# Optimization experiments

Measured on AMD Instinct MI355X. Metric: run time of the kernel, lower is better.

Reference implementation:

```python
import jax, jax.numpy as jnp
import numpy as np


def conv2d_same(x, w, b=None):
    # x: [B,C,H,W], w: [O,I,kh,kw], stride 1, SAME padding (pad=1 for 3x3)
    out = jax.lax.conv_general_dilated(
        x, w, window_strides=(1, 1), padding='SAME',
        dimension_numbers=('NCHW', 'OIHW', 'NCHW'))
    if b is not None:
        out = out + b[None, :, None, None]
    return out


def deform_conv(x, offset, wd, k=3, pad=1, dg=4):
    # DCNv1: per-location offset-guided bilinear sampling + weighted accumulation.
    # x: [B,C,H,W]; offset: [B, dg*k*k*2, H, W] as (dy,dx) pairs per kernel tap;
    # wd: [O, C, k, k] (bias-free, as in mmcv DeformConv).
    B, C, H, W = x.shape
    cg = C // dg          # channels per deformable group
    K = k * k
    off = offset.reshape(B, dg, K, 2, H, W)
    dy, dx = off[:, :, :, 0], off[:, :, :, 1]          # [B,dg,K,H,W]
    ky = (jnp.arange(K) // k - pad).astype(x.dtype)    # kernel row offsets
    kx = (jnp.arange(K) % k - pad).astype(x.dtype)     # kernel col offsets
    hh = jnp.arange(H, dtype=x.dtype)
    ww = jnp.arange(W, dtype=x.dtype)
    py = dy + ky[None, None, :, None, None] + hh[None, None, None, :, None]
    px = dx + kx[None, None, :, None, None] + ww[None, None, None, None, :]
    y0 = jnp.floor(py); x0 = jnp.floor(px)
    wy1 = py - y0; wy0 = 1.0 - wy1
    wx1 = px - x0; wx0 = 1.0 - wx1
    xg = x.reshape(B, dg, cg, H * W)

    def gather(yi, xi):
        # zero outside the feature map (implicit zero padding of bilinear kernel)
        valid = (yi >= 0) & (yi < H) & (xi >= 0) & (xi < W)
        yc = jnp.clip(yi, 0, H - 1).astype(jnp.int32)
        xc = jnp.clip(xi, 0, W - 1).astype(jnp.int32)
        idx = (yc * W + xc).reshape(B, dg, 1, K * H * W)
        g = jnp.take_along_axis(xg, jnp.broadcast_to(idx, (B, dg, cg, K * H * W)), axis=-1)
        g = g.reshape(B, dg, cg, K, H, W)
        return g * valid[:, :, None].astype(x.dtype)

    val = (gather(y0, x0) * (wy0 * wx0)[:, :, None]
           + gather(y0, x0 + 1) * (wy0 * wx1)[:, :, None]
           + gather(y0 + 1, x0) * (wy1 * wx0)[:, :, None]
           + gather(y0 + 1, x0 + 1) * (wy1 * wx1)[:, :, None])  # [B,dg,cg,K,H,W]
    wr = wd.reshape(wd.shape[0], dg, cg, K)
    return jnp.einsum('ogck,bgckhw->bohw', wr, val)


def setup_inputs() -> dict:
    key = jax.random.key(0)
    k1, k2, k3, k4 = jax.random.split(key, 4)
    B, C, H, W = 8, 256, 64, 64
    dg, ks = 4, 3
    x = jax.random.normal(k1, (B, C, H, W), dtype=jnp.float32)
    w1 = jax.random.normal(k2, (C, C, 3, 3), dtype=jnp.float32) * 0.01
    b1 = jnp.zeros((C,), dtype=jnp.float32)
    w2 = jax.random.normal(k3, (dg * ks * ks * 2, C, 3, 3), dtype=jnp.float32) * 0.01
    b2 = jnp.zeros((dg * ks * ks * 2,), dtype=jnp.float32)
    wd = jax.random.normal(k4, (C, C, ks, ks), dtype=jnp.float32) * 0.01
    return {'x': x, 'w1': w1, 'b1': b1, 'w2': w2, 'b2': b2, 'wd': wd}


def reference(x, w1, b1, w2, b2, wd):
    # offset branch uses x.detach() in the original
    xd = jax.lax.stop_gradient(x)
    offset = conv2d_same(conv2d_same(xd, w1, b1), w2, b2)
    return jax.nn.relu(deform_conv(x, offset, wd, k=3, pad=1, dg=4))
```

## Files before the change

kernel.cpp:

```cpp
#include <hip/hip_runtime.h>
#include <hip/hip_bf16.h>


typedef __attribute__((ext_vector_type(8))) short bf16x8;
typedef __attribute__((ext_vector_type(4))) float f32x4;

static __device__ __forceinline__ ushort f2bf(float f) {
  __hip_bfloat16 h = __float2bfloat16(f);
  return *reinterpret_cast<ushort*>(&h);
}
static __device__ __forceinline__ float bf2f(ushort u) {
  union { uint u32; float f; } cv;
  cv.u32 = ((uint)u) << 16;
  return cv.f;
}

__global__ __launch_bounds__(256) void prep_weights(
    const float* __restrict__ w1, const float* __restrict__ w2,
    const float* __restrict__ wd,
    ushort* __restrict__ wt1s, ushort* __restrict__ wt2s,
    ushort* __restrict__ wtds) {
  const int N1 = 36 * 256 * 64;
  const int N2 = 36 * 80 * 64;
  const int N3 = 36 * 256 * 64;
  int total = N1 + N2 + N3;
  for (int i = blockIdx.x * 256 + threadIdx.x; i < total; i += gridDim.x * 256) {
    if (i < N1) {
      int e = i & 7, p = (i >> 3) & 7, co = (i >> 6) & 255, ti = i >> 14;
      int cc = ((p ^ (co & 7)) << 3) + e;
      int kk = ti >> 2, chunk = ti & 3;
      wt1s[i] = f2bf(w1[(co * 256 + chunk * 64 + cc) * 9 + kk]);
    } else if (i < N1 + N2) {
      int d = i - N1;
      int e = d & 7, p = (d >> 3) & 7;
      int r = d >> 6;
      int co = r % 80, ti = r / 80;
      int cc = ((p ^ (co & 7)) << 3) + e;
      int kk = ti >> 2, chunk = ti & 3;
      wt2s[d] = (co < 72) ? f2bf(w2[(co * 256 + chunk * 64 + cc) * 9 + kk])
                          : (ushort)0;
    } else {
      int d = i - N1 - N2;
      int e = d & 7, p = (d >> 3) & 7, co = (d >> 6) & 255, ti = d >> 14;
      int c = ((p ^ (co & 7)) << 3) + e;
      int g = ti / 9, kk = ti - g * 9;
      wtds[d] = f2bf(wd[(co * 256 + g * 64 + c) * 9 + kk]);
    }
  }
}

__global__ __launch_bounds__(256) void transpose_x(
    const float* __restrict__ x, ushort* __restrict__ xt) {
  int id = blockIdx.x;
  int y = id & 63, bg = id >> 6;
  int c = threadIdx.x & 63, xi = threadIdx.x >> 6;
  const float* ip = x + (((size_t)bg) << 18) + ((size_t)c << 12) + y * 64;
  ushort* op = xt + (((size_t)bg) << 18) + (size_t)y * 4096 + c;
#pragma unroll
  for (int j = 0; j < 16; ++j) {
    int xx = xi * 16 + j;
    op[(size_t)xx * 64] = f2bf(ip[xx]);
  }
}

template <int MODE, int NFR, bool RELU, bool HASBIAS, bool OUT_CHLAST>
__global__ __launch_bounds__(256, 2) void fa_mfma6(
    const ushort* __restrict__ inT,
    const float* __restrict__ off,
    const char* __restrict__ wBs,
    const float* __restrict__ bias,
    void* __restrict__ outp,
    int co_total, int co_write) {
  constexpr int CO_TILE = NFR * 16;
  constexpr int TILE_B = CO_TILE * 128;
  constexpr int NCALLS = (TILE_B + 4095) / 4096;
  constexpr int NRN = (MODE == 1) ? 8 : 2;
  __shared__ __align__(16) ushort Blds[2][NCALLS * 2048];

  int id = blockIdx.x;
  int id2 = (id & 7) * 64 + (id >> 3);
  int b = id2 >> 6, h = id2 & 63;
  int t = threadIdx.x;
  int wv = t >> 6, lane = t & 63;
  int ml = lane & 15, kc = lane >> 4;
  int ml7 = ml & 7;

  auto stage = [&](int ti, int bufsel) {
#pragma unroll
    for (int m = 0; m < NCALLS; ++m) {
      int d = (m * 256 + t) * 16;
      int ds = (d > TILE_B - 16) ? (TILE_B - 16) : d;
      const char* src = wBs + (size_t)ti * TILE_B + ds;
      ushort* dst = &Blds[bufsel][(m * 256 + t) * 8];
      __builtin_amdgcn_global_load_lds(
          (const __attribute__((address_space(1))) void*)src,
          (__attribute__((address_space(3))) void*)dst, 16, 0, 0);
    }
  };

  const int pcol = wv * 16 + ml;

  const bf16x8 bz = {0, 0, 0, 0, 0, 0, 0, 0};
  bf16x8 aCur[2];
  bf16x8 rN[NRN];
  float wsv[4];
  float2 offA;

  auto issueA0 = [&](int tn) {
    int kk = tn >> 2, chunk = tn & 3;
    int ky = kk / 3, kx = kk - ky * 3;
    int gy = h + ky - 1, gx = pcol + kx - 1;
    bool inb = (gy >= 0) & (gy < 64) & (gx >= 0) & (gx < 64);
    const ushort* p =
        inT + ((((size_t)(b * 4 + chunk) << 12) + gy * 64 + gx) << 6) + kc * 8;
    rN[0] = bz;
    rN[1] = bz;
    if (inb) {
      rN[0] = *(const bf16x8*)p;
      rN[1] = *(const bf16x8*)(p + 32);
    }
  };
  auto finishA0 = [&]() {
    aCur[0] = rN[0];
    aCur[1] = rN[1];
  };

  auto loadOff = [&](int tn) {
    int g = tn / 9, kk = tn - 9 * (tn / 9);
    int ch = g * 18 + kk * 2;
    const float* offp = off + (((size_t)b * 72 + ch) << 12) + h * 64 + pcol;
    offA.x = offp[0];
    offA.y = offp[4096];
  };
  auto issueA1 = [&](int tn) {
    int g = tn / 9, kk = tn - 9 * (tn / 9);
    int ky = kk / 3, kx = kk - ky * 3;
    const ushort* base = inT + (((size_t)(b * 4 + g)) << 18) + kc * 8;
    float py = (float)(h + ky - 1) + offA.x;
    float pxf = (float)(pcol + kx - 1) + offA.y;
    float y0f = floorf(py), x0f = floorf(pxf);
    float wy1 = py - y0f, wx1 = pxf - x0f;
    float wy0 = 1.f - wy1, wx0 = 1.f - wx1;
    int y0 = (int)y0f, x0i = (int)x0f;
    int y1 = y0 + 1, x1i = x0i + 1;
    bool vy0 = (y0 >= 0) & (y0 < 64);
    bool vy1 = (y1 >= 0) & (y1 < 64);
    bool vx0 = (x0i >= 0) & (x0i < 64);
    bool vx1 = (x1i >= 0) & (x1i < 64);
    wsv[0] = (vy0 & vx0) ? wy0 * wx0 : 0.f;
    wsv[1] = (vy0 & vx1) ? wy0 * wx1 : 0.f;
    wsv[2] = (vy1 & vx0) ? wy1 * wx0 : 0.f;
    wsv[3] = (vy1 & vx1) ? wy1 * wx1 : 0.f;
    int yc0 = min(max(y0, 0), 63), yc1 = min(max(y1, 0), 63);
    int xc0 = min(max(x0i, 0), 63), xc1 = min(max(x1i, 0), 63);
    const ushort* p00 = base + ((yc0 * 64 + xc0) << 6);
    const ushort* p01 = base + ((yc0 * 64 + xc1) << 6);
    const ushort* p10 = base + ((yc1 * 64 + xc0) << 6);
    const ushort* p11 = base + ((yc1 * 64 + xc1) << 6);
    rN[0] = *(const bf16x8*)p00;
    rN[1] = *(const bf16x8*)(p00 + 32);
    rN[2] = *(const bf16x8*)p01;
    rN[3] = *(const bf16x8*)(p01 + 32);
    rN[4] = *(const bf16x8*)p10;
    rN[5] = *(const bf16x8*)(p10 + 32);
    rN[6] = *(const bf16x8*)p11;
    rN[7] = *(const bf16x8*)(p11 + 32);
  };
  auto finishA1 = [&]() {
    float w00 = wsv[0], w01 = wsv[1], w10 = wsv[2], w11 = wsv[3];
#pragma unroll
    for (int ks = 0; ks < 2; ++ks) {
      bf16x8 q00 = rN[0 + ks], q01 = rN[2 + ks];
      bf16x8 q10 = rN[4 + ks], q11 = rN[6 + ks];
      bf16x8 av;
#pragma unroll
      for (int jj = 0; jj < 4; ++jj) {
        float v0 = w00 * bf2f((ushort)q00[2 * jj]) + w01 * bf2f((ushort)q01[2 * jj]) +
                   w10 * bf2f((ushort)q10[2 * jj]) + w11 * bf2f((ushort)q11[2 * jj]);
        float v1 = w00 * bf2f((ushort)q00[2 * jj + 1]) + w01 * bf2f((ushort)q01[2 * jj + 1]) +
                   w10 * bf2f((ushort)q10[2 * jj + 1]) + w11 * bf2f((ushort)q11[2 * jj + 1]);
        av[2 * jj] = (short)f2bf(v0);
        av[2 * jj + 1] = (short)f2bf(v1);
      }
      aCur[ks] = av;
    }
  };

  f32x4 acc[NFR];
#pragma unroll
  for (int j = 0; j < NFR; ++j) acc[j] = (f32x4){0.f, 0.f, 0.f, 0.f};

  if (MODE == 1) {
    loadOff(0);
    issueA1(0);
    loadOff(1);
    finishA1();
  } else {
    issueA0(0);
    finishA0();
  }
  stage(0, 0);
  __syncthreads();

  for (int ti = 0; ti < 36; ++ti) {
    int cur = ti & 1;
    if (ti < 35) {
      stage(ti + 1, cur ^ 1);
      if (MODE == 1) issueA1(ti + 1); else issueA0(ti + 1);
    }
    if (MODE == 1 && ti < 34) loadOff(ti + 2);

#pragma unroll
    for (int ks = 0; ks < 2; ++ks) {
      int sw = (((ks * 4 + kc) ^ ml7) << 3);
      bf16x8 bq[NFR];
#pragma unroll
      for (int nf = 0; nf < NFR; ++nf)
        bq[nf] = *(const bf16x8*)&Blds[cur][(nf * 16 + ml) * 64 + sw];
#pragma unroll
      for (int nf = 0; nf < NFR; ++nf)
        acc[nf] = __builtin_amdgcn_mfma_f32_16x16x32_bf16(
            aCur[ks], bq[nf], acc[nf], 0, 0, 0);
    }

    if (ti < 35) { if (MODE == 1) finishA1(); else finishA0(); }
    __syncthreads();
  }

  int rq = lane >> 4;
#pragma unroll
  for (int nf = 0; nf < NFR; ++nf) {
    int cog = nf * 16 + ml;
    if (cog < co_write) {
      float bv = HASBIAS ? bias[cog] : 0.f;
#pragma unroll
      for (int ri = 0; ri < 4; ++ri) {
        int pxe = wv * 16 + rq * 4 + ri;
        float v = acc[nf][ri] + bv;
        if (RELU) v = fmaxf(v, 0.f);
        if (OUT_CHLAST) {
          int g_out = cog >> 6, ci = cog & 63;
          ((ushort*)outp)[((((size_t)(b * 4 + g_out) << 12) + h * 64 + pxe) << 6) + ci] =
              f2bf(v);
        } else {
          ((float*)outp)[(((size_t)b * co_total + cog) << 12) + h * 64 + pxe] = v;
        }
      }
    }
  }
}

extern "C" void kernel_launch(void* const* d_in, const int* in_sizes, int n_in,
                              void* d_out, int out_size, void* d_ws, size_t ws_size,
                              hipStream_t stream) {
  const float* x  = (const float*)d_in[0];
  const float* w1 = (const float*)d_in[1];
  const float* b1 = (const float*)d_in[2];
  const float* w2 = (const float*)d_in[3];
  const float* b2 = (const float*)d_in[4];
  const float* wd = (const float*)d_in[5];

  char* wsb = (char*)d_ws;
  float*  off_buf = (float*)wsb;
  ushort* xt      = (ushort*)(wsb + 9437184);
  ushort* wt1s    = (ushort*)(wsb + 26214400);
  ushort* wt2s    = (ushort*)(wsb + 27394048);
  ushort* wtds    = (ushort*)(wsb + 27762688);

  prep_weights<<<2048, 256, 0, stream>>>(w1, w2, wd, wt1s, wt2s, wtds);
  transpose_x<<<2048, 256, 0, stream>>>(x, xt);

  fa_mfma6<0, 16, false, true, true>
      <<<512, 256, 0, stream>>>(xt, nullptr, (const char*)wt1s, b1, d_out, 256, 256);

  fa_mfma6<0, 5, false, true, false>
      <<<512, 256, 0, stream>>>((const ushort*)d_out, nullptr, (const char*)wt2s,
                                b2, off_buf, 72, 72);

  fa_mfma6<1, 16, true, false, false>
      <<<512, 256, 0, stream>>>(xt, off_buf, (const char*)wtds, nullptr, d_out,
                                256, 256);
}
```

Baseline: 189.1 us.

## Split K dimension across blocks with bf16 partials and separate reduce kernels

Each conv/deform-conv kernel now uses 512-thread blocks covering two output rows, and splits the 36 K-steps into two halves handled by different blocks. Each half writes bf16 partial sums to a workspace buffer, and three new reduce kernels combine them and apply bias, ReLU and the final layout transpose. The kernel also raises wave priority around the MFMA section. In exchange it adds extra launches and partial-buffer traffic, and storing partials in bf16 loses accuracy.

```diff
diff --git a/kernel.cpp b/kernel.cpp
--- a/kernel.cpp
+++ b/kernel.cpp
@@ -63,42 +63,47 @@
   }
 }
 
-template <int MODE, int NFR, bool RELU, bool HASBIAS, bool OUT_CHLAST>
-__global__ __launch_bounds__(256, 2) void fa_mfma6(
+template <int MODE, int NFR, bool CHLAST>
+__global__ __launch_bounds__(512, 4) void fa_mfma8(
     const ushort* __restrict__ inT,
     const float* __restrict__ off,
     const char* __restrict__ wBs,
-    const float* __restrict__ bias,
-    void* __restrict__ outp,
-    int co_total, int co_write) {
+    ushort* __restrict__ parA,
+    ushort* __restrict__ parB,
+    int co_write) {
   constexpr int CO_TILE = NFR * 16;
   constexpr int TILE_B = CO_TILE * 128;
-  constexpr int NCALLS = (TILE_B + 4095) / 4096;
+  constexpr int NCALLS = (TILE_B + 8191) / 8192;
   constexpr int NRN = (MODE == 1) ? 8 : 2;
-  __shared__ __align__(16) ushort Blds[2][NCALLS * 2048];
+  __shared__ __align__(16) ushort Blds[2][NCALLS * 4096];
 
   int id = blockIdx.x;
   int id2 = (id & 7) * 64 + (id >> 3);
-  int b = id2 >> 6, h = id2 & 63;
+  int khalf = id2 & 1;
+  int rest = id2 >> 1;
+  int hp = rest & 31, b = rest >> 5;
   int t = threadIdx.x;
   int wv = t >> 6, lane = t & 63;
   int ml = lane & 15, kc = lane >> 4;
   int ml7 = ml & 7;
-
-  auto stage = [&](int ti, int bufsel) {
+  ushort* par = khalf ? parB : parA;
+
+  auto stage = [&](int tg, int bufsel) {
 #pragma unroll
     for (int m = 0; m < NCALLS; ++m) {
-      int d = (m * 256 + t) * 16;
+      int d = (m * 512 + t) * 16;
       int ds = (d > TILE_B - 16) ? (TILE_B - 16) : d;
-      const char* src = wBs + (size_t)ti * TILE_B + ds;
-      ushort* dst = &Blds[bufsel][(m * 256 + t) * 8];
+      const char* src = wBs + (size_t)tg * TILE_B + ds;
+      ushort* dst = &Blds[bufsel][(m * 512 + t) * 8];
       __builtin_amdgcn_global_load_lds(
           (const __attribute__((address_space(1))) void*)src,
           (__attribute__((address_space(3))) void*)dst, 16, 0, 0);
     }
   };
 
-  const int pcol = wv * 16 + ml;
+  const int pxll = wv * 16 + ml;
+  const int row = hp * 2 + (pxll >> 6);
+  const int col = pxll & 63;
 
   const bf16x8 bz = {0, 0, 0, 0, 0, 0, 0, 0};
   bf16x8 aCur[2];
@@ -106,10 +111,10 @@
   float wsv[4];
   float2 offA;
 
-  auto issueA0 = [&](int tn) {
-    int kk = tn >> 2, chunk = tn & 3;
+  auto issueA0 = [&](int tg) {
+    int kk = tg >> 2, chunk = tg & 3;
     int ky = kk / 3, kx = kk - ky * 3;
-    int gy = h + ky - 1, gx = pcol + kx - 1;
+    int gy = row + ky - 1, gx = col + kx - 1;
     bool inb = (gy >= 0) & (gy < 64) & (gx >= 0) & (gx < 64);
     const ushort* p =
         inT + ((((size_t)(b * 4 + chunk) << 12) + gy * 64 + gx) << 6) + kc * 8;
@@ -125,19 +130,19 @@
     aCur[1] = rN[1];
   };
 
-  auto loadOff = [&](int tn) {
-    int g = tn / 9, kk = tn - 9 * (tn / 9);
+  auto loadOff = [&](int tg) {
+    int g = tg / 9, kk = tg - 9 * (tg / 9);
     int ch = g * 18 + kk * 2;
-    const float* offp = off + (((size_t)b * 72 + ch) << 12) + h * 64 + pcol;
+    const float* offp = off + (((size_t)b * 72 + ch) << 12) + row * 64 + col;
     offA.x = offp[0];
     offA.y = offp[4096];
   };
-  auto issueA1 = [&](int tn) {
-    int g = tn / 9, kk = tn - 9 * (tn / 9);
+  auto issueA1 = [&](int tg) {
+    int g = tg / 9, kk = tg - 9 * (tg / 9);
     int ky = kk / 3, kx = kk - ky * 3;
     const ushort* base = inT + (((size_t)(b * 4 + g)) << 18) + kc * 8;
-    float py = (float)(h + ky - 1) + offA.x;
-    float pxf = (float)(pcol + kx - 1) + offA.y;
+    float py = (float)(row + ky - 1) + offA.x;
+    float pxf = (float)(col + kx - 1) + offA.y;
     float y0f = floorf(py), x0f = floorf(pxf);
     float wy1 = py - y0f, wx1 = pxf - x0f;
     float wy0 = 1.f - wy1, wx0 = 1.f - wx1;
@@ -190,26 +195,30 @@
 #pragma unroll
   for (int j = 0; j < NFR; ++j) acc[j] = (f32x4){0.f, 0.f, 0.f, 0.f};
 
+  const int t0 = khalf * 18;
+
   if (MODE == 1) {
-    loadOff(0);
-    issueA1(0);
-    loadOff(1);
+    loadOff(t0);
+    issueA1(t0);
+    loadOff(t0 + 1);
     finishA1();
   } else {
-    issueA0(0);
+    issueA0(t0);
     finishA0();
   }
-  stage(0, 0);
+  stage(t0, 0);
   __syncthreads();
 
-  for (int ti = 0; ti < 36; ++ti) {
-    int cur = ti & 1;
-    if (ti < 35) {
-      stage(ti + 1, cur ^ 1);
-      if (MODE == 1) issueA1(ti + 1); else issueA0(ti + 1);
-    }
-    if (MODE == 1 && ti < 34) loadOff(ti + 2);
-
+  for (int tloc = 0; tloc < 18; ++tloc) {
+    int tg = t0 + tloc;
+    int cur = tloc & 1;
+    if (tloc < 17) {
+      stage(tg + 1, cur ^ 1);
+      if (MODE == 1) issueA1(tg + 1); else issueA0(tg + 1);
+    }
+    if (MODE == 1 && tloc < 16) loadOff(tg + 2);
+
+    __builtin_amdgcn_s_setprio(1);
 #pragma unroll
     for (int ks = 0; ks < 2; ++ks) {
       int sw = (((ks * 4 + kc) ^ ml7) << 3);
@@ -222,8 +231,9 @@
         acc[nf] = __builtin_amdgcn_mfma_f32_16x16x32_bf16(
             aCur[ks], bq[nf], acc[nf], 0, 0, 0);
     }
-
-    if (ti < 35) { if (MODE == 1) finishA1(); else finishA0(); }
+    __builtin_amdgcn_s_setprio(0);
+
+    if (tloc < 17) { if (MODE == 1) finishA1(); else finishA0(); }
     __syncthreads();
   }
 
@@ -232,21 +242,86 @@
   for (int nf = 0; nf < NFR; ++nf) {
     int cog = nf * 16 + ml;
     if (cog < co_write) {
-      float bv = HASBIAS ? bias[cog] : 0.f;
 #pragma unroll
       for (int ri = 0; ri < 4; ++ri) {
-        int pxe = wv * 16 + rq * 4 + ri;
-        float v = acc[nf][ri] + bv;
-        if (RELU) v = fmaxf(v, 0.f);
-        if (OUT_CHLAST) {
-          int g_out = cog >> 6, ci = cog & 63;
-          ((ushort*)outp)[((((size_t)(b * 4 + g_out) << 12) + h * 64 + pxe) << 6) + ci] =
-              f2bf(v);
+        int pix = hp * 128 + wv * 16 + rq * 4 + ri;
+        ushort v = f2bf(acc[nf][ri]);
+        if (CHLAST) {
+          par[((((size_t)(b * 4 + (cog >> 6)) << 12) + pix) << 6) + (cog & 63)] = v;
         } else {
-          ((float*)outp)[(((size_t)b * co_total + cog) << 12) + h * 64 + pxe] = v;
+          par[(((size_t)b * co_write + cog) << 12) + pix] = v;
         }
       }
     }
+  }
+}
+
+__global__ __launch_bounds__(256) void reduce_c1(
+    const ushort* __restrict__ p0, const ushort* __restrict__ p1,
+    const float* __restrict__ bias, ushort* __restrict__ t1) {
+  const int N8 = (8 * 4 * 4096 * 64) / 8;
+  for (int i = blockIdx.x * 256 + threadIdx.x; i < N8; i += gridDim.x * 256) {
+    size_t base = (size_t)i * 8;
+    bf16x8 a = *(const bf16x8*)(p0 + base);
+    bf16x8 c = *(const bf16x8*)(p1 + base);
+    int c0 = (int)(base & 63);
+    int g = (int)((base >> 18) & 3);
+    bf16x8 o;
+#pragma unroll
+    for (int j = 0; j < 8; ++j) {
+      float v = bf2f((ushort)a[j]) + bf2f((ushort)c[j]) + bias[g * 64 + c0 + j];
+      o[j] = (short)f2bf(v);
+    }
+    *(bf16x8*)(t1 + base) = o;
+  }
+}
+
+__global__ __launch_bounds__(256) void reduce_c2(
+    const ushort* __restrict__ p0, const ushort* __restrict__ p1,
+    const float* __restrict__ bias, float* __restrict__ out) {
+  const int N8 = (8 * 72 * 4096) / 8;
+  for (int i = blockIdx.x * 256 + threadIdx.x; i < N8; i += gridDim.x * 256) {
+    size_t base = (size_t)i * 8;
+    bf16x8 a = *(const bf16x8*)(p0 + base);
+    bf16x8 c = *(const bf16x8*)(p1 + base);
+    int co = (int)((base >> 12) % 72);
+    float bv = bias[co];
+    float4 o0, o1;
+    o0.x = bf2f((ushort)a[0]) + bf2f((ushort)c[0]) + bv;
+    o0.y = bf2f((ushort)a[1]) + bf2f((ushort)c[1]) + bv;
+    o0.z = bf2f((ushort)a[2]) + bf2f((ushort)c[2]) + bv;
+    o0.w = bf2f((ushort)a[3]) + bf2f((ushort)c[3]) + bv;
+    o1.x = bf2f((ushort)a[4]) + bf2f((ushort)c[4]) + bv;
+    o1.y = bf2f((ushort)a[5]) + bf2f((ushort)c[5]) + bv;
+    o1.z = bf2f((ushort)a[6]) + bf2f((ushort)c[6]) + bv;
+    o1.w = bf2f((ushort)a[7]) + bf2f((ushort)c[7]) + bv;
+    *(float4*)(out + base) = o0;
+    *(float4*)(out + base + 4) = o1;
+  }
+}
+
+__global__ __launch_bounds__(256) void reduce_df(
+    const ushort* __restrict__ p0, const ushort* __restrict__ p1,
+    float* __restrict__ out) {
+  __shared__ float ts[64][65];
+  int bid = blockIdx.x;
+  int pt = bid & 63, cq = (bid >> 6) & 3, b = bid >> 8;
+  int t = threadIdx.x;
+  int c = t & 63, ty = t >> 6;
+  size_t inbase = (((size_t)(b * 4 + cq) << 12) + pt * 64) << 6;
+#pragma unroll 4
+  for (int s = 0; s < 16; ++s) {
+    int pxi = ty * 16 + s;
+    size_t idx = inbase + ((size_t)pxi << 6) + c;
+    float v = bf2f(p0[idx]) + bf2f(p1[idx]);
+    ts[c][pxi] = fmaxf(v, 0.f);
+  }
+  __syncthreads();
+  int px = t & 63;
+#pragma unroll 4
+  for (int s = 0; s < 16; ++s) {
+    int coi = ty * 16 + s;
+    out[(((size_t)b * 256 + cq * 64 + coi) << 12) + pt * 64 + px] = ts[coi][px];
   }
 }
 
@@ -266,18 +341,23 @@
   ushort* wt1s    = (ushort*)(wsb + 26214400);
   ushort* wt2s    = (ushort*)(wsb + 27394048);
   ushort* wtds    = (ushort*)(wsb + 27762688);
+  ushort* par0    = (ushort*)(wsb + 28942336);
+  ushort* par1    = (ushort*)(wsb + 45719552);
 
   prep_weights<<<2048, 256, 0, stream>>>(w1, w2, wd, wt1s, wt2s, wtds);
   transpose_x<<<2048, 256, 0, stream>>>(x, xt);
 
-  fa_mfma6<0, 16, false, true, true>
-      <<<512, 256, 0, stream>>>(xt, nullptr, (const char*)wt1s, b1, d_out, 256, 256);
-
-  fa_mfma6<0, 5, false, true, false>
-      <<<512, 256, 0, stream>>>((const ushort*)d_out, nullptr, (const char*)wt2s,
-                                b2, off_buf, 72, 72);
-
-  fa_mfma6<1, 16, true, false, false>
-      <<<512, 256, 0, stream>>>(xt, off_buf, (const char*)wtds, nullptr, d_out,
-                                256, 256);
-}
+  ushort* t1 = (ushort*)d_out;
+
+  fa_mfma8<0, 16, true><<<512, 512, 0, stream>>>(
+      xt, nullptr, (const char*)wt1s, par0, par1, 256);
+  reduce_c1<<<2048, 256, 0, stream>>>(par0, par1, b1, t1);
+
+  fa_mfma8<0, 5, false><<<512, 512, 0, stream>>>(
+      t1, nullptr, (const char*)wt2s, par0, par1, 72);
+  reduce_c2<<<1024, 256, 0, stream>>>(par0, par1, b2, off_buf);
+
+  fa_mfma8<1, 16, true><<<512, 512, 0, stream>>>(
+      xt, off_buf, (const char*)wtds, par0, par1, 256);
+  reduce_df<<<2048, 256, 0, stream>>>(par0, par1, (float*)d_out);
+}
```

Result: slower. 208.8 us (+10.4%).

## Split reduction dimension across two blocks with partial buffers and reduce kernels

Applied to the files above, without the earlier changes.

Each GEMM-like kernel is split along the 36-step reduction into two halves, doubling the grid to 1024 blocks. Each half writes bf16 partial sums that new reduce kernels combine, adding bias and ReLU. Weight tiles are re-laid out into per-half-k sub-tiles without swizzle, shrinking LDS and allowing 3 blocks per SM, and MFMA sections are wrapped with setprio. The aim is more occupancy and parallelism at the cost of extra partial-sum traffic, three extra launches, and an extra bf16 rounding of the partial sums.

```diff
diff --git a/kernel.cpp b/kernel.cpp
--- a/kernel.cpp
+++ b/kernel.cpp
@@ -18,33 +18,34 @@
 __global__ __launch_bounds__(256) void prep_weights(
     const float* __restrict__ w1, const float* __restrict__ w2,
     const float* __restrict__ wd,
-    ushort* __restrict__ wt1s, ushort* __restrict__ wt2s,
-    ushort* __restrict__ wtds) {
-  const int N1 = 36 * 256 * 64;
-  const int N2 = 36 * 80 * 64;
-  const int N3 = 36 * 256 * 64;
+    ushort* __restrict__ wt1, ushort* __restrict__ wt2,
+    ushort* __restrict__ wtd) {
+  const int N1 = 72 * 4 * 256 * 8;
+  const int N2 = 72 * 4 * 128 * 8;
+  const int N3 = 72 * 4 * 256 * 8;
   int total = N1 + N2 + N3;
   for (int i = blockIdx.x * 256 + threadIdx.x; i < total; i += gridDim.x * 256) {
     if (i < N1) {
-      int e = i & 7, p = (i >> 3) & 7, co = (i >> 6) & 255, ti = i >> 14;
-      int cc = ((p ^ (co & 7)) << 3) + e;
-      int kk = ti >> 2, chunk = ti & 3;
-      wt1s[i] = f2bf(w1[(co * 256 + chunk * 64 + cc) * 9 + kk]);
+      int e = i & 7, co = (i >> 3) & 255, p = (i >> 11) & 3, tk = i >> 13;
+      int ti = tk >> 1, half = tk & 1;
+      int kk = ti >> 2, ch = ti & 3;
+      int cc = half * 32 + p * 8 + e;
+      wt1[i] = f2bf(w1[(co * 256 + ch * 64 + cc) * 9 + kk]);
     } else if (i < N1 + N2) {
       int d = i - N1;
-      int e = d & 7, p = (d >> 3) & 7;
-      int r = d >> 6;
-      int co = r % 80, ti = r / 80;
-      int cc = ((p ^ (co & 7)) << 3) + e;
-      int kk = ti >> 2, chunk = ti & 3;
-      wt2s[d] = (co < 72) ? f2bf(w2[(co * 256 + chunk * 64 + cc) * 9 + kk])
-                          : (ushort)0;
+      int e = d & 7, co = (d >> 3) & 127, p = (d >> 10) & 3, tk = d >> 12;
+      int ti = tk >> 1, half = tk & 1;
+      int kk = ti >> 2, ch = ti & 3;
+      int cc = half * 32 + p * 8 + e;
+      wt2[d] = (co < 72) ? f2bf(w2[(co * 256 + ch * 64 + cc) * 9 + kk])
+                         : (ushort)0;
     } else {
       int d = i - N1 - N2;
-      int e = d & 7, p = (d >> 3) & 7, co = (d >> 6) & 255, ti = d >> 14;
-      int c = ((p ^ (co & 7)) << 3) + e;
-      int g = ti / 9, kk = ti - g * 9;
-      wtds[d] = f2bf(wd[(co * 256 + g * 64 + c) * 9 + kk]);
+      int e = d & 7, co = (d >> 3) & 255, p = (d >> 11) & 3, tk = d >> 13;
+      int ti = tk >> 1, half = tk & 1;
+      int g = ti / 9, kkt = ti - g * 9;
+      int c = half * 32 + p * 8 + e;
+      wtd[d] = f2bf(wd[(co * 256 + g * 64 + c) * 9 + kkt]);
     }
   }
 }
@@ -63,51 +64,50 @@
   }
 }
 
-template <int MODE, int NFR, bool RELU, bool HASBIAS, bool OUT_CHLAST>
-__global__ __launch_bounds__(256, 2) void fa_mfma6(
+template <int MODE, int NFR>
+__global__ __launch_bounds__(256, 3) void fa_mfma10(
     const ushort* __restrict__ inT,
     const float* __restrict__ off,
-    const char* __restrict__ wBs,
-    const float* __restrict__ bias,
-    void* __restrict__ outp,
-    int co_total, int co_write) {
+    const ushort* __restrict__ wBs,
+    ushort* __restrict__ parA,
+    ushort* __restrict__ parB) {
   constexpr int CO_TILE = NFR * 16;
-  constexpr int TILE_B = CO_TILE * 128;
-  constexpr int NCALLS = (TILE_B + 4095) / 4096;
+  constexpr int SUB_U = CO_TILE * 32;
+  constexpr int NCALLS = (SUB_U * 2) / 4096;
   constexpr int NRN = (MODE == 1) ? 8 : 2;
-  __shared__ __align__(16) ushort Blds[2][NCALLS * 2048];
+  __shared__ __align__(16) ushort Blds[2][SUB_U];
 
   int id = blockIdx.x;
-  int id2 = (id & 7) * 64 + (id >> 3);
-  int b = id2 >> 6, h = id2 & 63;
+  int id2 = (id & 7) * 128 + (id >> 3);
+  int khalf = id2 & 1;
+  int rest = id2 >> 1;
+  int h = rest & 63, b = rest >> 6;
   int t = threadIdx.x;
   int wv = t >> 6, lane = t & 63;
   int ml = lane & 15, kc = lane >> 4;
-  int ml7 = ml & 7;
-
-  auto stage = [&](int ti, int bufsel) {
+  int pcol = wv * 16 + ml;
+  ushort* par = khalf ? parB : parA;
+
+  auto stage = [&](int s, int buf) {
+    int tk = khalf * 36 + s;
+    const char* src0 = (const char*)wBs + (size_t)tk * (SUB_U * 2) + t * 16;
+    ushort* dst0 = &Blds[buf][t * 8];
 #pragma unroll
     for (int m = 0; m < NCALLS; ++m) {
-      int d = (m * 256 + t) * 16;
-      int ds = (d > TILE_B - 16) ? (TILE_B - 16) : d;
-      const char* src = wBs + (size_t)ti * TILE_B + ds;
-      ushort* dst = &Blds[bufsel][(m * 256 + t) * 8];
       __builtin_amdgcn_global_load_lds(
-          (const __attribute__((address_space(1))) void*)src,
-          (__attribute__((address_space(3))) void*)dst, 16, 0, 0);
-    }
-  };
-
-  const int pcol = wv * 16 + ml;
+          (const __attribute__((address_space(1))) void*)(src0 + m * 4096),
+          (__attribute__((address_space(3))) void*)(dst0 + m * 2048), 16, 0, 0);
+    }
+  };
 
   const bf16x8 bz = {0, 0, 0, 0, 0, 0, 0, 0};
-  bf16x8 aCur[2];
+  bf16x8 aCur0, aCur1;
   bf16x8 rN[NRN];
   float wsv[4];
   float2 offA;
 
-  auto issueA0 = [&](int tn) {
-    int kk = tn >> 2, chunk = tn & 3;
+  auto issueA0 = [&](int tap) {
+    int kk = tap >> 2, chunk = tap & 3;
     int ky = kk / 3, kx = kk - ky * 3;
     int gy = h + ky - 1, gx = pcol + kx - 1;
     bool inb = (gy >= 0) & (gy < 64) & (gx >= 0) & (gx < 64);
@@ -121,20 +121,20 @@
     }
   };
   auto finishA0 = [&]() {
-    aCur[0] = rN[0];
-    aCur[1] = rN[1];
-  };
-
-  auto loadOff = [&](int tn) {
-    int g = tn / 9, kk = tn - 9 * (tn / 9);
-    int ch = g * 18 + kk * 2;
+    aCur0 = rN[0];
+    aCur1 = rN[1];
+  };
+
+  auto loadOff = [&](int tap) {
+    int g = tap / 9, kkt = tap - 9 * (tap / 9);
+    int ch = g * 18 + kkt * 2;
     const float* offp = off + (((size_t)b * 72 + ch) << 12) + h * 64 + pcol;
     offA.x = offp[0];
     offA.y = offp[4096];
   };
-  auto issueA1 = [&](int tn) {
-    int g = tn / 9, kk = tn - 9 * (tn / 9);
-    int ky = kk / 3, kx = kk - ky * 3;
+  auto issueA1 = [&](int tap) {
+    int g = tap / 9, kkt = tap - 9 * (tap / 9);
+    int ky = kkt / 3, kx = kkt - ky * 3;
     const ushort* base = inT + (((size_t)(b * 4 + g)) << 18) + kc * 8;
     float py = (float)(h + ky - 1) + offA.x;
     float pxf = (float)(pcol + kx - 1) + offA.y;
@@ -174,15 +174,12 @@
       bf16x8 q10 = rN[4 + ks], q11 = rN[6 + ks];
       bf16x8 av;
 #pragma unroll
-      for (int jj = 0; jj < 4; ++jj) {
-        float v0 = w00 * bf2f((ushort)q00[2 * jj]) + w01 * bf2f((ushort)q01[2 * jj]) +
-                   w10 * bf2f((ushort)q10[2 * jj]) + w11 * bf2f((ushort)q11[2 * jj]);
-        float v1 = w00 * bf2f((ushort)q00[2 * jj + 1]) + w01 * bf2f((ushort)q01[2 * jj + 1]) +
-                   w10 * bf2f((ushort)q10[2 * jj + 1]) + w11 * bf2f((ushort)q11[2 * jj + 1]);
-        av[2 * jj] = (short)f2bf(v0);
-        av[2 * jj + 1] = (short)f2bf(v1);
+      for (int jj = 0; jj < 8; ++jj) {
+        float v = w00 * bf2f((ushort)q00[jj]) + w01 * bf2f((ushort)q01[jj]) +
+                  w10 * bf2f((ushort)q10[jj]) + w11 * bf2f((ushort)q11[jj]);
+        av[jj] = (short)f2bf(v);
       }
-      aCur[ks] = av;
+      if (ks == 0) aCur0 = av; else aCur1 = av;
     }
   };
 
@@ -190,63 +187,122 @@
 #pragma unroll
   for (int j = 0; j < NFR; ++j) acc[j] = (f32x4){0.f, 0.f, 0.f, 0.f};
 
+  auto domfma = [&](bf16x8 a, int buf) {
+    __builtin_amdgcn_s_setprio(1);
+#pragma unroll
+    for (int nf = 0; nf < NFR; ++nf) {
+      bf16x8 bq = *(const bf16x8*)&Blds[buf][(kc * CO_TILE + nf * 16 + ml) * 8];
+      acc[nf] = __builtin_amdgcn_mfma_f32_16x16x32_bf16(a, bq, acc[nf], 0, 0, 0);
+    }
+    __builtin_amdgcn_s_setprio(0);
+  };
+
+  const int tap0 = khalf * 18;
+
   if (MODE == 1) {
-    loadOff(0);
-    issueA1(0);
-    loadOff(1);
+    loadOff(tap0);
+    issueA1(tap0);
+    loadOff(tap0 + 1);
     finishA1();
   } else {
-    issueA0(0);
+    issueA0(tap0);
     finishA0();
   }
   stage(0, 0);
   __syncthreads();
 
-  for (int ti = 0; ti < 36; ++ti) {
-    int cur = ti & 1;
-    if (ti < 35) {
-      stage(ti + 1, cur ^ 1);
-      if (MODE == 1) issueA1(ti + 1); else issueA0(ti + 1);
-    }
-    if (MODE == 1 && ti < 34) loadOff(ti + 2);
-
-#pragma unroll
-    for (int ks = 0; ks < 2; ++ks) {
-      int sw = (((ks * 4 + kc) ^ ml7) << 3);
-      bf16x8 bq[NFR];
-#pragma unroll
-      for (int nf = 0; nf < NFR; ++nf)
-        bq[nf] = *(const bf16x8*)&Blds[cur][(nf * 16 + ml) * 64 + sw];
-#pragma unroll
-      for (int nf = 0; nf < NFR; ++nf)
-        acc[nf] = __builtin_amdgcn_mfma_f32_16x16x32_bf16(
-            aCur[ks], bq[nf], acc[nf], 0, 0, 0);
-    }
-
-    if (ti < 35) { if (MODE == 1) finishA1(); else finishA0(); }
+  for (int tp = 0; tp < 18; ++tp) {
+    int tap = tap0 + tp;
+    if (2 * tp + 1 < 36) stage(2 * tp + 1, 1);
+    if (tp < 17) { if (MODE == 1) issueA1(tap + 1); else issueA0(tap + 1); }
+    if (MODE == 1 && tp < 16) loadOff(tap + 2);
+    domfma(aCur0, 0);
     __syncthreads();
-  }
-
-  int rq = lane >> 4;
-#pragma unroll
-  for (int nf = 0; nf < NFR; ++nf) {
-    int cog = nf * 16 + ml;
-    if (cog < co_write) {
-      float bv = HASBIAS ? bias[cog] : 0.f;
-#pragma unroll
-      for (int ri = 0; ri < 4; ++ri) {
-        int pxe = wv * 16 + rq * 4 + ri;
-        float v = acc[nf][ri] + bv;
-        if (RELU) v = fmaxf(v, 0.f);
-        if (OUT_CHLAST) {
-          int g_out = cog >> 6, ci = cog & 63;
-          ((ushort*)outp)[((((size_t)(b * 4 + g_out) << 12) + h * 64 + pxe) << 6) + ci] =
-              f2bf(v);
-        } else {
-          ((float*)outp)[(((size_t)b * co_total + cog) << 12) + h * 64 + pxe] = v;
-        }
-      }
-    }
+    if (2 * tp + 2 < 36) stage(2 * tp + 2, 0);
+    domfma(aCur1, 1);
+    if (tp < 17) { if (MODE == 1) finishA1(); else finishA0(); }
+    __syncthreads();
+  }
+
+  size_t wbase = ((size_t)((b * 64 + h) * 4 + wv)) * (NFR * 4 * 64);
+#pragma unroll
+  for (int nf = 0; nf < NFR; ++nf)
+#pragma unroll
+    for (int ri = 0; ri < 4; ++ri)
+      par[wbase + (nf * 4 + ri) * 64 + lane] = f2bf(acc[nf][ri]);
+}
+
+
+__global__ __launch_bounds__(256) void reduce_c1(
+    const ushort* __restrict__ p0, const ushort* __restrict__ p1,
+    const float* __restrict__ bias, ushort* __restrict__ t1) {
+  const int N = 8 * 4 * 4096 * 8;
+  for (int i = blockIdx.x * 256 + threadIdx.x; i < N; i += gridDim.x * 256) {
+    int cg = i & 7;
+    int pix = (i >> 3) & 4095;
+    int g = (i >> 15) & 3;
+    int b = i >> 17;
+    int h = pix >> 6, col = pix & 63;
+    int wv = col >> 4, rr = col & 15;
+    int rq = rr >> 2, ri = rr & 3;
+    int cp = g * 64 + cg * 8;
+    int nf = cp >> 4, mlb = cp & 15;
+    size_t idx = ((size_t)((b * 64 + h) * 4 + wv)) * 4096 +
+                 (nf * 4 + ri) * 64 + rq * 16 + mlb;
+    bf16x8 a = *(const bf16x8*)(p0 + idx);
+    bf16x8 c = *(const bf16x8*)(p1 + idx);
+    bf16x8 o;
+#pragma unroll
+    for (int j = 0; j < 8; ++j)
+      o[j] = (short)f2bf(bf2f((ushort)a[j]) + bf2f((ushort)c[j]) + bias[cp + j]);
+    *(bf16x8*)(t1 + ((size_t)(b * 4 + g) * 4096 + pix) * 64 + cg * 8) = o;
+  }
+}
+
+__global__ __launch_bounds__(256) void reduce_c2(
+    const ushort* __restrict__ p0, const ushort* __restrict__ p1,
+    const float* __restrict__ bias, float* __restrict__ out) {
+  const int N = 8 * 72 * 1024;
+  for (int i = blockIdx.x * 256 + threadIdx.x; i < N; i += gridDim.x * 256) {
+    int p4 = i & 1023;
+    int r = i >> 10;
+    int co = r % 72, b = r / 72;
+    int h = p4 >> 4;
+    int col0 = (p4 & 15) * 4;
+    int wv = col0 >> 4, rq = (col0 >> 2) & 3;
+    int nf = co >> 4, ml = co & 15;
+    size_t base = ((size_t)((b * 64 + h) * 4 + wv)) * 2048 +
+                  nf * 256 + rq * 16 + ml;
+    float bv = bias[co];
+    float4 o;
+    o.x = bf2f(p0[base +   0]) + bf2f(p1[base +   0]) + bv;
+    o.y = bf2f(p0[base +  64]) + bf2f(p1[base +  64]) + bv;
+    o.z = bf2f(p0[base + 128]) + bf2f(p1[base + 128]) + bv;
+    o.w = bf2f(p0[base + 192]) + bf2f(p1[base + 192]) + bv;
+    *(float4*)(out + (((size_t)b * 72 + co) << 12) + p4 * 4) = o;
+  }
+}
+
+__global__ __launch_bounds__(256) void reduce_df(
+    const ushort* __restrict__ p0, const ushort* __restrict__ p1,
+    float* __restrict__ out) {
+  const int N = 8 * 256 * 1024;
+  for (int i = blockIdx.x * 256 + threadIdx.x; i < N; i += gridDim.x * 256) {
+    int p4 = i & 1023;
+    int co = (i >> 10) & 255;
+    int b = i >> 18;
+    int h = p4 >> 4;
+    int col0 = (p4 & 15) * 4;
+    int wv = col0 >> 4, rq = (col0 >> 2) & 3;
+    int nf = co >> 4, ml = co & 15;
+    size_t base = ((size_t)((b * 64 + h) * 4 + wv)) * 4096 +
+                  nf * 256 + rq * 16 + ml;
+    float4 o;
+    o.x = fmaxf(bf2f(p0[base +   0]) + bf2f(p1[base +   0]), 0.f);
+    o.y = fmaxf(bf2f(p0[base +  64]) + bf2f(p1[base +  64]), 0.f);
+    o.z = fmaxf(bf2f(p0[base + 128]) + bf2f(p1[base + 128]), 0.f);
+    o.w = fmaxf(bf2f(p0[base + 192]) + bf2f(p1[base + 192]), 0.f);
+    *(float4*)(out + (((size_t)b * 256 + co) << 12) + p4 * 4) = o;
   }
 }
 
@@ -263,21 +319,23 @@
   char* wsb = (char*)d_ws;
   float*  off_buf = (float*)wsb;
   ushort* xt      = (ushort*)(wsb + 9437184);
-  ushort* wt1s    = (ushort*)(wsb + 26214400);
-  ushort* wt2s    = (ushort*)(wsb + 27394048);
-  ushort* wtds    = (ushort*)(wsb + 27762688);
-
-  prep_weights<<<2048, 256, 0, stream>>>(w1, w2, wd, wt1s, wt2s, wtds);
+  ushort* wt1     = (ushort*)(wsb + 26214400);
+  ushort* wt2     = (ushort*)(wsb + 27394048);
+  ushort* wtd     = (ushort*)(wsb + 27983872);
+  ushort* par0    = (ushort*)(wsb + 29163520);
+  ushort* par1    = (ushort*)(wsb + 45940736);
+
+  prep_weights<<<2048, 256, 0, stream>>>(w1, w2, wd, wt1, wt2, wtd);
   transpose_x<<<2048, 256, 0, stream>>>(x, xt);
 
-  fa_mfma6<0, 16, false, true, true>
-      <<<512, 256, 0, stream>>>(xt, nullptr, (const char*)wt1s, b1, d_out, 256, 256);
-
-  fa_mfma6<0, 5, false, true, false>
-      <<<512, 256, 0, stream>>>((const ushort*)d_out, nullptr, (const char*)wt2s,
-                                b2, off_buf, 72, 72);
-
-  fa_mfma6<1, 16, true, false, false>
-      <<<512, 256, 0, stream>>>(xt, off_buf, (const char*)wtds, nullptr, d_out,
-                                256, 256);
-}
+  ushort* t1 = (ushort*)d_out;
+
+  fa_mfma10<0, 16><<<1024, 256, 0, stream>>>(xt, nullptr, wt1, par0, par1);
+  reduce_c1<<<2048, 256, 0, stream>>>(par0, par1, b1, t1);
+
+  fa_mfma10<0, 8><<<1024, 256, 0, stream>>>(t1, nullptr, wt2, par0, par1);
+  reduce_c2<<<1024, 256, 0, stream>>>(par0, par1, b2, off_buf);
+
+  fa_mfma10<1, 16><<<1024, 256, 0, stream>>>(xt, off_buf, wtd, par0, par1);
+  reduce_df<<<2048, 256, 0, stream>>>(par0, par1, (float*)d_out);
+}
```

Result: slower. 236.2 us (+24.9%).

## Re-tile first conv so each wave covers all pixels and a quarter of channels

Applied to the files above, without the earlier changes.

The kernel gets a template parameter for the number of pixel fragments per wave (MFR). The first 3x3 conv uses MFR=4 with each wave owning 64 of the 256 output channels across all 64 pixels, instead of 16 pixels across all channels. This cuts the LDS B-fragment reads per wave by four at the cost of four times the A-fragment global loads per wave and more registers. It also adds s_setprio around the MFMA block to favour matrix issue over other waves.

```diff
diff --git a/kernel.cpp b/kernel.cpp
--- a/kernel.cpp
+++ b/kernel.cpp
@@ -63,15 +63,15 @@
   }
 }
 
-template <int MODE, int NFR, bool RELU, bool HASBIAS, bool OUT_CHLAST>
-__global__ __launch_bounds__(256, 2) void fa_mfma6(
+template <int MODE, int MFR, int NFR, int CO_TILE, bool RELU, bool HASBIAS,
+          bool OUT_CHLAST>
+__global__ __launch_bounds__(256, 2) void fa_mfma13(
     const ushort* __restrict__ inT,
     const float* __restrict__ off,
     const char* __restrict__ wBs,
     const float* __restrict__ bias,
     void* __restrict__ outp,
     int co_total, int co_write) {
-  constexpr int CO_TILE = NFR * 16;
   constexpr int TILE_B = CO_TILE * 128;
   constexpr int NCALLS = (TILE_B + 4095) / 4096;
   constexpr int NRN = (MODE == 1) ? 8 : 2;
@@ -84,6 +84,8 @@
   int wv = t >> 6, lane = t & 63;
   int ml = lane & 15, kc = lane >> 4;
   int ml7 = ml & 7;
+
+  const int cobw = (MFR == 4) ? wv * (NFR * 16) : 0;
 
   auto stage = [&](int ti, int bufsel) {
 #pragma unroll
@@ -98,37 +100,48 @@
     }
   };
 
-  const int pcol = wv * 16 + ml;
+  int pcol[MFR];
+#pragma unroll
+  for (int mf = 0; mf < MFR; ++mf)
+    pcol[mf] = ((MFR == 1) ? wv * 16 : mf * 16) + ml;
 
   const bf16x8 bz = {0, 0, 0, 0, 0, 0, 0, 0};
-  bf16x8 aCur[2];
-  bf16x8 rN[NRN];
+  bf16x8 aCur[MFR][2];
+  bf16x8 rN[MFR][NRN];
   float wsv[4];
   float2 offA;
 
   auto issueA0 = [&](int tn) {
     int kk = tn >> 2, chunk = tn & 3;
     int ky = kk / 3, kx = kk - ky * 3;
-    int gy = h + ky - 1, gx = pcol + kx - 1;
-    bool inb = (gy >= 0) & (gy < 64) & (gx >= 0) & (gx < 64);
-    const ushort* p =
-        inT + ((((size_t)(b * 4 + chunk) << 12) + gy * 64 + gx) << 6) + kc * 8;
-    rN[0] = bz;
-    rN[1] = bz;
-    if (inb) {
-      rN[0] = *(const bf16x8*)p;
-      rN[1] = *(const bf16x8*)(p + 32);
+    int gy = h + ky - 1;
+    bool rowok = (gy >= 0) & (gy < 64);
+#pragma unroll
+    for (int mf = 0; mf < MFR; ++mf) {
+      int gx = pcol[mf] + kx - 1;
+      bool inb = rowok & (gx >= 0) & (gx < 64);
+      const ushort* p =
+          inT + ((((size_t)(b * 4 + chunk) << 12) + gy * 64 + gx) << 6) + kc * 8;
+      rN[mf][0] = bz;
+      rN[mf][1] = bz;
+      if (inb) {
+        rN[mf][0] = *(const bf16x8*)p;
+        rN[mf][1] = *(const bf16x8*)(p + 32);
+      }
     }
   };
   auto finishA0 = [&]() {
-    aCur[0] = rN[0];
-    aCur[1] = rN[1];
+#pragma unroll
+    for (int mf = 0; mf < MFR; ++mf) {
+      aCur[mf][0] = rN[mf][0];
+      aCur[mf][1] = rN[mf][1];
+    }
   };
 
   auto loadOff = [&](int tn) {
     int g = tn / 9, kk = tn - 9 * (tn / 9);
     int ch = g * 18 + kk * 2;
-    const float* offp = off + (((size_t)b * 72 + ch) << 12) + h * 64 + pcol;
+    const float* offp = off + (((size_t)b * 72 + ch) << 12) + h * 64 + pcol[0];
     offA.x = offp[0];
     offA.y = offp[4096];
   };
@@ -137,7 +150,7 @@
     int ky = kk / 3, kx = kk - ky * 3;
     const ushort* base = inT + (((size_t)(b * 4 + g)) << 18) + kc * 8;
     float py = (float)(h + ky - 1) + offA.x;
-    float pxf = (float)(pcol + kx - 1) + offA.y;
+    float pxf = (float)(pcol[0] + kx - 1) + offA.y;
     float y0f = floorf(py), x0f = floorf(pxf);
     float wy1 = py - y0f, wx1 = pxf - x0f;
     float wy0 = 1.f - wy1, wx0 = 1.f - wx1;
@@ -157,21 +170,21 @@
     const ushort* p01 = base + ((yc0 * 64 + xc1) << 6);
     const ushort* p10 = base + ((yc1 * 64 + xc0) << 6);
     const ushort* p11 = base + ((yc1 * 64 + xc1) << 6);
-    rN[0] = *(const bf16x8*)p00;
-    rN[1] = *(const bf16x8*)(p00 + 32);
-    rN[2] = *(const bf16x8*)p01;
-    rN[3] = *(const bf16x8*)(p01 + 32);
-    rN[4] = *(const bf16x8*)p10;
-    rN[5] = *(const bf16x8*)(p10 + 32);
-    rN[6] = *(const bf16x8*)p11;
-    rN[7] = *(const bf16x8*)(p11 + 32);
+    rN[0][0] = *(const bf16x8*)p00;
+    rN[0][1] = *(const bf16x8*)(p00 + 32);
+    rN[0][2] = *(const bf16x8*)p01;
+    rN[0][3] = *(const bf16x8*)(p01 + 32);
+    rN[0][4] = *(const bf16x8*)p10;
+    rN[0][5] = *(const bf16x8*)(p10 + 32);
+    rN[0][6] = *(const bf16x8*)p11;
+    rN[0][7] = *(const bf16x8*)(p11 + 32);
   };
   auto finishA1 = [&]() {
     float w00 = wsv[0], w01 = wsv[1], w10 = wsv[2], w11 = wsv[3];
 #pragma unroll
     for (int ks = 0; ks < 2; ++ks) {
-      bf16x8 q00 = rN[0 + ks], q01 = rN[2 + ks];
-      bf16x8 q10 = rN[4 + ks], q11 = rN[6 + ks];
+      bf16x8 q00 = rN[0][0 + ks], q01 = rN[0][2 + ks];
+      bf16x8 q10 = rN[0][4 + ks], q11 = rN[0][6 + ks];
       bf16x8 av;
 #pragma unroll
       for (int jj = 0; jj < 4; ++jj) {
@@ -182,13 +195,15 @@
         av[2 * jj] = (short)f2bf(v0);
         av[2 * jj + 1] = (short)f2bf(v1);
       }
-      aCur[ks] = av;
-    }
-  };
-
-  f32x4 acc[NFR];
-#pragma unroll
-  for (int j = 0; j < NFR; ++j) acc[j] = (f32x4){0.f, 0.f, 0.f, 0.f};
+      aCur[0][ks] = av;
+    }
+  };
+
+  f32x4 acc[MFR][NFR];
+#pragma unroll
+  for (int i = 0; i < MFR; ++i)
+#pragma unroll
+    for (int j = 0; j < NFR; ++j) acc[i][j] = (f32x4){0.f, 0.f, 0.f, 0.f};
 
   if (MODE == 1) {
     loadOff(0);
@@ -210,18 +225,22 @@
     }
     if (MODE == 1 && ti < 34) loadOff(ti + 2);
 
+    __builtin_amdgcn_s_setprio(1);
 #pragma unroll
     for (int ks = 0; ks < 2; ++ks) {
       int sw = (((ks * 4 + kc) ^ ml7) << 3);
       bf16x8 bq[NFR];
 #pragma unroll
       for (int nf = 0; nf < NFR; ++nf)
-        bq[nf] = *(const bf16x8*)&Blds[cur][(nf * 16 + ml) * 64 + sw];
-#pragma unroll
-      for (int nf = 0; nf < NFR; ++nf)
-        acc[nf] = __builtin_amdgcn_mfma_f32_16x16x32_bf16(
-            aCur[ks], bq[nf], acc[nf], 0, 0, 0);
-    }
+        bq[nf] = *(const bf16x8*)&Blds[cur][(cobw + nf * 16 + ml) * 64 + sw];
+#pragma unroll
+      for (int mf = 0; mf < MFR; ++mf)
+#pragma unroll
+        for (int nf = 0; nf < NFR; ++nf)
+          acc[mf][nf] = __builtin_amdgcn_mfma_f32_16x16x32_bf16(
+              aCur[mf][ks], bq[nf], acc[mf][nf], 0, 0, 0);
+    }
+    __builtin_amdgcn_s_setprio(0);
 
     if (ti < 35) { if (MODE == 1) finishA1(); else finishA0(); }
     __syncthreads();
@@ -230,20 +249,23 @@
   int rq = lane >> 4;
 #pragma unroll
   for (int nf = 0; nf < NFR; ++nf) {
-    int cog = nf * 16 + ml;
+    int cog = cobw + nf * 16 + ml;
     if (cog < co_write) {
       float bv = HASBIAS ? bias[cog] : 0.f;
 #pragma unroll
-      for (int ri = 0; ri < 4; ++ri) {
-        int pxe = wv * 16 + rq * 4 + ri;
-        float v = acc[nf][ri] + bv;
-        if (RELU) v = fmaxf(v, 0.f);
-        if (OUT_CHLAST) {
-          int g_out = cog >> 6, ci = cog & 63;
-          ((ushort*)outp)[((((size_t)(b * 4 + g_out) << 12) + h * 64 + pxe) << 6) + ci] =
-              f2bf(v);
-        } else {
-          ((float*)outp)[(((size_t)b * co_total + cog) << 12) + h * 64 + pxe] = v;
+      for (int mf = 0; mf < MFR; ++mf) {
+#pragma unroll
+        for (int ri = 0; ri < 4; ++ri) {
+          int pxe = ((MFR == 1) ? wv * 16 : mf * 16) + rq * 4 + ri;
+          float v = acc[mf][nf][ri] + bv;
+          if (RELU) v = fmaxf(v, 0.f);
+          if (OUT_CHLAST) {
+            int g_out = cog >> 6, ci = cog & 63;
+            ((ushort*)outp)[((((size_t)(b * 4 + g_out) << 12) + h * 64 + pxe) << 6) + ci] =
+                f2bf(v);
+          } else {
+            ((float*)outp)[(((size_t)b * co_total + cog) << 12) + h * 64 + pxe] = v;
+          }
         }
       }
     }
@@ -270,14 +292,16 @@
   prep_weights<<<2048, 256, 0, stream>>>(w1, w2, wd, wt1s, wt2s, wtds);
   transpose_x<<<2048, 256, 0, stream>>>(x, xt);
 
-  fa_mfma6<0, 16, false, true, true>
-      <<<512, 256, 0, stream>>>(xt, nullptr, (const char*)wt1s, b1, d_out, 256, 256);
-
-  fa_mfma6<0, 5, false, true, false>
-      <<<512, 256, 0, stream>>>((const ushort*)d_out, nullptr, (const char*)wt2s,
-                                b2, off_buf, 72, 72);
-
-  fa_mfma6<1, 16, true, false, false>
+  ushort* t1 = (ushort*)d_out;
+
+  fa_mfma13<0, 4, 4, 256, false, true, true>
+      <<<512, 256, 0, stream>>>(xt, nullptr, (const char*)wt1s, b1, t1, 256, 256);
+
+  fa_mfma13<0, 1, 5, 80, false, true, false>
+      <<<512, 256, 0, stream>>>(t1, nullptr, (const char*)wt2s, b2,
+                                off_buf, 72, 72);
+
+  fa_mfma13<1, 1, 16, 256, true, false, false>
       <<<512, 256, 0, stream>>>(xt, off_buf, (const char*)wtds, nullptr, d_out,
                                 256, 256);
 }
```

After: 216.1 us. 1.14x slower.
